# Kernel optimization log

Hardware: AMD Instinct MI355X
Metric: run time of the kernel (lower is better)

The kernel has to match this reference:

```python
import jax, jax.numpy as jnp
import numpy as np

NUM_CLASSES = 19
EPS_MEAN = 1e-6
EPS_COS = 1e-8


def setup_inputs() -> dict:
    key = jax.random.key(0)
    k1, k2, k3 = jax.random.split(key, 3)
    B, C, H, W = 8, 256, 96, 192
    feat_S = jax.random.normal(k1, (B, C, H, W), dtype=jnp.float32)
    feat_T = jax.random.normal(k2, (B, C, H, W), dtype=jnp.float32)
    target = jax.random.randint(k3, (B, H, W), 0, NUM_CLASSES, dtype=jnp.int32)
    return {"feat_S": feat_S, "feat_T": feat_T, "target": target}


def _class_centers(feat, target, num_classes):
    # feat: [B,C,H,W], target: [B,H,W] int labels
    # Per-(batch, class) mean over masked pixels; pixels keep their own
    # feature if their label is outside [0, num_classes) (masks are disjoint,
    # so the sequential per-class overwrite loop == a single segment-mean).
    onehot = (target[:, None, :, :] == jnp.arange(num_classes)[None, :, None, None]).astype(feat.dtype)  # [B,K,H,W]
    sums = jnp.einsum('bkhw,bchw->bkc', onehot, feat)           # [B,K,C]
    counts = jnp.sum(onehot, axis=(2, 3))                        # [B,K]
    means = sums / (counts[..., None] + EPS_MEAN)                # [B,K,C]
    B, C, H, W = feat.shape
    idx = jnp.clip(target, 0, num_classes - 1).reshape(B, H * W)  # [B,HW]
    gathered = jnp.take_along_axis(means, idx[:, :, None], axis=1)  # [B,HW,C]
    center = jnp.transpose(gathered.reshape(B, H, W, C), (0, 3, 1, 2))  # [B,C,H,W]
    valid = ((target >= 0) & (target < num_classes))[:, None, :, :]
    return jnp.where(valid, center, feat)


def _cos_sim_c(x, y):
    # cosine similarity along channel dim (dim=1), torch-style eps clamp
    dot = jnp.sum(x * y, axis=1)
    nx = jnp.sqrt(jnp.sum(x * x, axis=1))
    ny = jnp.sqrt(jnp.sum(y * y, axis=1))
    return dot / jnp.maximum(nx * ny, EPS_COS)


def reference(feat_S, feat_T, target):
    # feat_S already at feat_T resolution (bilinear resize is identity here);
    # target already at feature resolution (nearest upsample is identity).
    center_S = _class_centers(feat_S, target, NUM_CLASSES)
    center_T = _class_centers(feat_T, target, NUM_CLASSES)
    pcsim_S = _cos_sim_c(feat_S, center_S)  # [B,H,W]
    pcsim_T = _cos_sim_c(feat_T, center_T)  # [B,H,W]
    loss = jnp.mean((pcsim_S - pcsim_T) ** 2)
    return loss
```

## Files before the change

kernel.cpp:

```cpp
#include <hip/hip_runtime.h>

#define B 8
#define C 256
#define HW 18432
#define K 19
#define EPS_MEAN 1e-6f
#define EPS_COS 1e-8f
#define PAD 257

__global__ __launch_bounds__(256) void k_counts(const int* __restrict__ target,
                                                int* __restrict__ counts) {
    __shared__ int hist[K * 256];
    __shared__ int red[K][4];
    const int tid = threadIdx.x, b = blockIdx.x;
    for (int k = 0; k < K; ++k) hist[k * 256 + tid] = 0;
    const int4* t4 = (const int4*)(target + b * HW);
    for (int i = 0; i < HW / 1024; ++i) {
        int4 t = t4[i * 256 + tid];
        if ((unsigned)t.x < K) hist[t.x * 256 + tid]++;
        if ((unsigned)t.y < K) hist[t.y * 256 + tid]++;
        if ((unsigned)t.z < K) hist[t.z * 256 + tid]++;
        if ((unsigned)t.w < K) hist[t.w * 256 + tid]++;
    }
    __syncthreads();
    const int wid = tid >> 6, lane = tid & 63;
    for (int k = 0; k < K; ++k) {
        int v = hist[k * 256 + tid];
        for (int off = 32; off; off >>= 1) v += __shfl_xor(v, off);
        if (lane == 0) red[k][wid] = v;
    }
    __syncthreads();
    if (tid < K) counts[b * K + tid] = red[tid][0] + red[tid][1] + red[tid][2] + red[tid][3];
}

__global__ __launch_bounds__(256) void k_sums(const float* __restrict__ fS,
                                              const float* __restrict__ fT,
                                              const int* __restrict__ target,
                                              float* __restrict__ sums) {
    __shared__ float hist[K * 256];
    __shared__ float red[K][4];
    const int tid = threadIdx.x;
    const int c = blockIdx.x, b = blockIdx.y, z = blockIdx.z;
    const float* feat = z ? fT : fS;
    for (int k = 0; k < K; ++k) hist[k * 256 + tid] = 0.0f;
    const float4* f4 = (const float4*)(feat + (size_t)(b * C + c) * HW);
    const int4*   t4 = (const int4*)(target + b * HW);
    for (int i = 0; i < HW / 1024; ++i) {
        float4 v = f4[i * 256 + tid];
        int4   t = t4[i * 256 + tid];
        if ((unsigned)t.x < K) hist[t.x * 256 + tid] += v.x;
        if ((unsigned)t.y < K) hist[t.y * 256 + tid] += v.y;
        if ((unsigned)t.z < K) hist[t.z * 256 + tid] += v.z;
        if ((unsigned)t.w < K) hist[t.w * 256 + tid] += v.w;
    }
    __syncthreads();
    const int wid = tid >> 6, lane = tid & 63;
    for (int k = 0; k < K; ++k) {
        float v = hist[k * 256 + tid];
        for (int off = 32; off; off >>= 1) v += __shfl_xor(v, off);
        if (lane == 0) red[k][wid] = v;
    }
    __syncthreads();
    if (tid < K)
        sums[((size_t)(z * B + b) * K + tid) * C + c] =
            red[tid][0] + red[tid][1] + red[tid][2] + red[tid][3];
}

__global__ __launch_bounds__(256) void k_means(const float* __restrict__ sums,
                                               const int* __restrict__ counts,
                                               float* __restrict__ means,
                                               float* __restrict__ ny) {
    __shared__ float red0[4], red1[4];
    const int tid = threadIdx.x;
    const int bk = blockIdx.x;
    const float inv = 1.0f / ((float)counts[bk] + EPS_MEAN);
    const size_t i0 = (size_t)bk * C + tid;
    const size_t i1 = (size_t)(B * K + bk) * C + tid;
    float m0 = sums[i0] * inv, m1 = sums[i1] * inv;
    means[i0] = m0; means[i1] = m1;
    float s0 = m0 * m0, s1 = m1 * m1;
    for (int off = 32; off; off >>= 1) {
        s0 += __shfl_xor(s0, off);
        s1 += __shfl_xor(s1, off);
    }
    const int wid = tid >> 6, lane = tid & 63;
    if (lane == 0) { red0[wid] = s0; red1[wid] = s1; }
    __syncthreads();
    if (tid == 0) ny[bk]         = sqrtf(red0[0] + red0[1] + red0[2] + red0[3]);
    if (tid == 1) ny[B * K + bk] = sqrtf(red1[0] + red1[1] + red1[2] + red1[3]);
}

__global__ __launch_bounds__(256) void k_loss(const float* __restrict__ fS,
                                              const float* __restrict__ fT,
                                              const int* __restrict__ target,
                                              const float* __restrict__ means,
                                              const float* __restrict__ ny,
                                              float* __restrict__ loss_acc) {
    __shared__ float mS[K * PAD];
    __shared__ float mT[K * PAD];
    __shared__ float nys[2 * K];
    __shared__ float red[4];
    const int tid = threadIdx.x;
    const int b = blockIdx.y;
    for (int idx = tid; idx < K * C; idx += 256) {
        int k = idx >> 8, c = idx & 255;
        mS[k * PAD + c] = means[((size_t)b * K + k) * C + c];
        mT[k * PAD + c] = means[((size_t)(B * K + b * K + k)) * C + c];
    }
    if (tid < 2 * K)
        nys[tid] = ny[(tid < K) ? (b * K + tid) : (B * K + b * K + (tid - K))];
    __syncthreads();

    const int px = blockIdx.x * 256 + tid;
    const int k = target[b * HW + px];
    const bool valid = (unsigned)k < (unsigned)K;
    const int kk = valid ? k : 0;
    const float* pS = fS + (size_t)b * C * HW + px;
    const float* pT = fT + (size_t)b * C * HW + px;
    const float* msrow = &mS[kk * PAD];
    const float* mtrow = &mT[kk * PAD];
    float dS = 0.f, qS = 0.f, dT = 0.f, qT = 0.f;
#pragma unroll 4
    for (int c = 0; c < C; ++c) {
        float vS = pS[(size_t)c * HW];
        float vT = pT[(size_t)c * HW];
        dS += vS * msrow[c]; qS += vS * vS;
        dT += vT * mtrow[c]; qT += vT * vT;
    }
    float psS = dS / fmaxf(sqrtf(qS) * nys[kk], EPS_COS);
    float psT = dT / fmaxf(sqrtf(qT) * nys[K + kk], EPS_COS);
    float d = valid ? (psS - psT) : 0.0f;
    float v = d * d;
    for (int off = 32; off; off >>= 1) v += __shfl_xor(v, off);
    const int wid = tid >> 6, lane = tid & 63;
    if (lane == 0) red[wid] = v;
    __syncthreads();
    if (tid == 0) atomicAdd(loss_acc, red[0] + red[1] + red[2] + red[3]);
}

__global__ void k_final(const float* __restrict__ loss_acc, float* __restrict__ out) {
    out[0] = loss_acc[0] * (1.0f / (float)(B * HW));
}

extern "C" void kernel_launch(void* const* d_in, const int* in_sizes, int n_in,
                              void* d_out, int out_size, void* d_ws, size_t ws_size,
                              hipStream_t stream) {
    const float* fS     = (const float*)d_in[0];
    const float* fT     = (const float*)d_in[1];
    const int*   target = (const int*)d_in[2];
    float* out = (float*)d_out;
    char*  ws  = (char*)d_ws;

    float* loss_acc = (float*)ws;
    float* sums     = (float*)(ws + 64);
    float* means    = (float*)(ws + 64 + 311296);
    int*   counts   = (int*)  (ws + 64 + 622592);
    float* ny       = (float*)(ws + 64 + 622592 + 1024);

    hipMemsetAsync(loss_acc, 0, 4, stream);
    k_counts<<<B, 256, 0, stream>>>(target, counts);
    k_sums<<<dim3(C, B, 2), 256, 0, stream>>>(fS, fT, target, sums);
    k_means<<<B * K, 256, 0, stream>>>(sums, counts, means, ny);
    k_loss<<<dim3(HW / 256, B), 256, 0, stream>>>(fS, fT, target, means, ny, loss_acc);
    k_final<<<1, 1, 0, stream>>>(loss_acc, out);
}
```

Measured before the change: 401.1 us.

## Split channel reduction across lane groups and parallelize class-count histogram

k_loss now runs 512-thread blocks in which each wavefront covers 16 pixels. Four lane groups each handle 64 channels, and their partial dot products and norms are combined with cross-lane shuffles. The aim is more memory-level parallelism per pixel, at the cost of 64-byte row segments instead of fully coalesced 256-pixel rows. k_counts is split into 9 blocks per batch that merge their results with global atomics into a zeroed workspace region. In k_sums and k_counts, the branchy histogram updates are replaced with branchless LDS atomics and an unroll pragma is added. Those atomics are unnecessary because each thread owns its own column, so they may add overhead.

```diff
diff --git a/kernel.cpp b/kernel.cpp
--- a/kernel.cpp
+++ b/kernel.cpp
@@ -12,17 +12,17 @@
                                                 int* __restrict__ counts) {
     __shared__ int hist[K * 256];
     __shared__ int red[K][4];
-    const int tid = threadIdx.x, b = blockIdx.x;
+    const int tid = threadIdx.x, cx = blockIdx.x, b = blockIdx.y;
     for (int k = 0; k < K; ++k) hist[k * 256 + tid] = 0;
-    const int4* t4 = (const int4*)(target + b * HW);
-    for (int i = 0; i < HW / 1024; ++i) {
+    const int4* t4 = (const int4*)(target + (size_t)b * HW + cx * 2048);
+#pragma unroll
+    for (int i = 0; i < 2; ++i) {
         int4 t = t4[i * 256 + tid];
-        if ((unsigned)t.x < K) hist[t.x * 256 + tid]++;
-        if ((unsigned)t.y < K) hist[t.y * 256 + tid]++;
-        if ((unsigned)t.z < K) hist[t.z * 256 + tid]++;
-        if ((unsigned)t.w < K) hist[t.w * 256 + tid]++;
+        { unsigned k0 = (unsigned)t.x; bool ok = k0 < K; atomicAdd(&hist[(ok ? k0 : 0u) * 256 + tid], ok ? 1 : 0); }
+        { unsigned k0 = (unsigned)t.y; bool ok = k0 < K; atomicAdd(&hist[(ok ? k0 : 0u) * 256 + tid], ok ? 1 : 0); }
+        { unsigned k0 = (unsigned)t.z; bool ok = k0 < K; atomicAdd(&hist[(ok ? k0 : 0u) * 256 + tid], ok ? 1 : 0); }
+        { unsigned k0 = (unsigned)t.w; bool ok = k0 < K; atomicAdd(&hist[(ok ? k0 : 0u) * 256 + tid], ok ? 1 : 0); }
     }
-    __syncthreads();
     const int wid = tid >> 6, lane = tid & 63;
     for (int k = 0; k < K; ++k) {
         int v = hist[k * 256 + tid];
@@ -30,7 +30,7 @@
         if (lane == 0) red[k][wid] = v;
     }
     __syncthreads();
-    if (tid < K) counts[b * K + tid] = red[tid][0] + red[tid][1] + red[tid][2] + red[tid][3];
+    if (tid < K) atomicAdd(&counts[b * K + tid], red[tid][0] + red[tid][1] + red[tid][2] + red[tid][3]);
 }
 
 __global__ __launch_bounds__(256) void k_sums(const float* __restrict__ fS,
@@ -44,16 +44,16 @@
     const float* feat = z ? fT : fS;
     for (int k = 0; k < K; ++k) hist[k * 256 + tid] = 0.0f;
     const float4* f4 = (const float4*)(feat + (size_t)(b * C + c) * HW);
-    const int4*   t4 = (const int4*)(target + b * HW);
+    const int4*   t4 = (const int4*)(target + (size_t)b * HW);
+#pragma unroll 4
     for (int i = 0; i < HW / 1024; ++i) {
         float4 v = f4[i * 256 + tid];
         int4   t = t4[i * 256 + tid];
-        if ((unsigned)t.x < K) hist[t.x * 256 + tid] += v.x;
-        if ((unsigned)t.y < K) hist[t.y * 256 + tid] += v.y;
-        if ((unsigned)t.z < K) hist[t.z * 256 + tid] += v.z;
-        if ((unsigned)t.w < K) hist[t.w * 256 + tid] += v.w;
+        { unsigned k0 = (unsigned)t.x; bool ok = k0 < K; atomicAdd(&hist[(ok ? k0 : 0u) * 256 + tid], ok ? v.x : 0.f); }
+        { unsigned k0 = (unsigned)t.y; bool ok = k0 < K; atomicAdd(&hist[(ok ? k0 : 0u) * 256 + tid], ok ? v.y : 0.f); }
+        { unsigned k0 = (unsigned)t.z; bool ok = k0 < K; atomicAdd(&hist[(ok ? k0 : 0u) * 256 + tid], ok ? v.z : 0.f); }
+        { unsigned k0 = (unsigned)t.w; bool ok = k0 < K; atomicAdd(&hist[(ok ? k0 : 0u) * 256 + tid], ok ? v.w : 0.f); }
     }
-    __syncthreads();
     const int wid = tid >> 6, lane = tid & 63;
     for (int k = 0; k < K; ++k) {
         float v = hist[k * 256 + tid];
@@ -90,7 +90,7 @@
     if (tid == 1) ny[B * K + bk] = sqrtf(red1[0] + red1[1] + red1[2] + red1[3]);
 }
 
-__global__ __launch_bounds__(256) void k_loss(const float* __restrict__ fS,
+__global__ __launch_bounds__(512) void k_loss(const float* __restrict__ fS,
                                               const float* __restrict__ fT,
                                               const int* __restrict__ target,
                                               const float* __restrict__ means,
@@ -99,10 +99,10 @@
     __shared__ float mS[K * PAD];
     __shared__ float mT[K * PAD];
     __shared__ float nys[2 * K];
-    __shared__ float red[4];
+    __shared__ float red[8];
     const int tid = threadIdx.x;
     const int b = blockIdx.y;
-    for (int idx = tid; idx < K * C; idx += 256) {
+    for (int idx = tid; idx < K * C; idx += 512) {
         int k = idx >> 8, c = idx & 255;
         mS[k * PAD + c] = means[((size_t)b * K + k) * C + c];
         mT[k * PAD + c] = means[((size_t)(B * K + b * K + k)) * C + c];
@@ -111,31 +111,40 @@
         nys[tid] = ny[(tid < K) ? (b * K + tid) : (B * K + b * K + (tid - K))];
     __syncthreads();
 
-    const int px = blockIdx.x * 256 + tid;
-    const int k = target[b * HW + px];
+    const int wid = tid >> 6, lane = tid & 63;
+    const int pxl = lane & 15, cg = lane >> 4;
+    const int px = blockIdx.x * 128 + wid * 16 + pxl;
+    const int k = target[(size_t)b * HW + px];
     const bool valid = (unsigned)k < (unsigned)K;
     const int kk = valid ? k : 0;
-    const float* pS = fS + (size_t)b * C * HW + px;
-    const float* pT = fT + (size_t)b * C * HW + px;
-    const float* msrow = &mS[kk * PAD];
-    const float* mtrow = &mT[kk * PAD];
+    const float* pS = fS + ((size_t)b * C + cg * 64) * HW + px;
+    const float* pT = fT + ((size_t)b * C + cg * 64) * HW + px;
+    const float* msrow = &mS[kk * PAD + cg * 64];
+    const float* mtrow = &mT[kk * PAD + cg * 64];
     float dS = 0.f, qS = 0.f, dT = 0.f, qT = 0.f;
-#pragma unroll 4
-    for (int c = 0; c < C; ++c) {
-        float vS = pS[(size_t)c * HW];
-        float vT = pT[(size_t)c * HW];
-        dS += vS * msrow[c]; qS += vS * vS;
-        dT += vT * mtrow[c]; qT += vT * vT;
+#pragma unroll 8
+    for (int i = 0; i < 64; ++i) {
+        float vS = pS[(size_t)i * HW];
+        float vT = pT[(size_t)i * HW];
+        dS += vS * msrow[i]; qS += vS * vS;
+        dT += vT * mtrow[i]; qT += vT * vT;
     }
+    dS += __shfl_xor(dS, 16); dS += __shfl_xor(dS, 32);
+    qS += __shfl_xor(qS, 16); qS += __shfl_xor(qS, 32);
+    dT += __shfl_xor(dT, 16); dT += __shfl_xor(dT, 32);
+    qT += __shfl_xor(qT, 16); qT += __shfl_xor(qT, 32);
     float psS = dS / fmaxf(sqrtf(qS) * nys[kk], EPS_COS);
     float psT = dT / fmaxf(sqrtf(qT) * nys[K + kk], EPS_COS);
-    float d = valid ? (psS - psT) : 0.0f;
+    float d = (valid && cg == 0) ? (psS - psT) : 0.0f;
     float v = d * d;
     for (int off = 32; off; off >>= 1) v += __shfl_xor(v, off);
-    const int wid = tid >> 6, lane = tid & 63;
     if (lane == 0) red[wid] = v;
     __syncthreads();
-    if (tid == 0) atomicAdd(loss_acc, red[0] + red[1] + red[2] + red[3]);
+    if (tid == 0) {
+        float s = 0.f;
+        for (int w = 0; w < 8; ++w) s += red[w];
+        atomicAdd(loss_acc, s);
+    }
 }
 
 __global__ void k_final(const float* __restrict__ loss_acc, float* __restrict__ out) {
@@ -152,15 +161,15 @@
     char*  ws  = (char*)d_ws;
 
     float* loss_acc = (float*)ws;
-    float* sums     = (float*)(ws + 64);
-    float* means    = (float*)(ws + 64 + 311296);
-    int*   counts   = (int*)  (ws + 64 + 622592);
-    float* ny       = (float*)(ws + 64 + 622592 + 1024);
+    int*   counts   = (int*)  (ws + 4);
+    float* sums     = (float*)(ws + 1024);
+    float* means    = (float*)(ws + 1024 + 311296);
+    float* ny       = (float*)(ws + 1024 + 622592);
 
-    hipMemsetAsync(loss_acc, 0, 4, stream);
-    k_counts<<<B, 256, 0, stream>>>(target, counts);
+    hipMemsetAsync(ws, 0, 1024, stream);
+    k_counts<<<dim3(9, B), 256, 0, stream>>>(target, counts);
     k_sums<<<dim3(C, B, 2), 256, 0, stream>>>(fS, fT, target, sums);
     k_means<<<B * K, 256, 0, stream>>>(sums, counts, means, ny);
-    k_loss<<<dim3(HW / 256, B), 256, 0, stream>>>(fS, fT, target, means, ny, loss_acc);
+    k_loss<<<dim3(HW / 128, B), 512, 0, stream>>>(fS, fT, target, means, ny, loss_acc);
     k_final<<<1, 1, 0, stream>>>(loss_acc, out);
 }
```

Measured after the change: 663.8 us. 65.5% more time.
